# Kernel tuning notes

Measured on AMD Instinct MI355X. Metric: run time of the kernel, lower is better.

## Reference

```python
import jax, jax.numpy as jnp
import numpy as np

N = 20000
E = 320000
D_IN = 256
D = 128
H = 4
L = 2
NUM_CLASSES = 7
LN_EPS = 1e-5


def setup_inputs() -> dict:
    key = jax.random.key(0)
    ks = jax.random.split(key, 12)
    inp = {}
    inp["x"] = jax.random.normal(ks[0], (N, D_IN), dtype=jnp.float32)
    inp["edge_index"] = jax.random.randint(ks[1], (2, E), 0, N, dtype=jnp.int32)
    inp["W_in"] = jax.random.normal(ks[2], (D_IN, D), dtype=jnp.float32) / np.sqrt(D_IN)
    inp["b_in"] = jnp.zeros((D,), jnp.float32)
    inp["Wq"] = jax.random.normal(ks[3], (L, D, H * D), dtype=jnp.float32) / np.sqrt(D)
    inp["bq"] = jnp.zeros((L, H * D), jnp.float32)
    inp["Wk"] = jax.random.normal(ks[4], (L, D, H * D), dtype=jnp.float32) / np.sqrt(D)
    inp["bk"] = jnp.zeros((L, H * D), jnp.float32)
    inp["Wv"] = jax.random.normal(ks[5], (L, D, H * D), dtype=jnp.float32) / np.sqrt(D)
    inp["bv"] = jnp.zeros((L, H * D), jnp.float32)
    inp["Wskip"] = jax.random.normal(ks[6], (L, D, D), dtype=jnp.float32) / np.sqrt(D)
    inp["bskip"] = jnp.zeros((L, D), jnp.float32)
    inp["ln_g"] = jnp.ones((L, D), jnp.float32)
    inp["ln_b"] = jnp.zeros((L, D), jnp.float32)
    inp["Wc"] = jax.random.normal(ks[7], (D, NUM_CLASSES), dtype=jnp.float32) / np.sqrt(D)
    inp["bc"] = jnp.zeros((NUM_CLASSES,), jnp.float32)
    return inp


def degree_pe(edge_index):
    # degree of source nodes (edge_index[0]), then sinusoidal encoding of the degree
    deg = jax.ops.segment_sum(jnp.ones((E,), jnp.float32), edge_index[0], num_segments=N)
    i = jnp.arange(D, dtype=jnp.float32)
    freq = deg[:, None] / jnp.power(10000.0, i / D)[None, :]  # [N, D]
    return jnp.where((jnp.arange(D) % 2 == 0)[None, :], jnp.sin(freq), jnp.cos(freq))


def transformer_conv(xf, edge_index, Wq, bq, Wk, bk, Wv, bv, Wskip, bskip):
    # PyG TransformerConv: heads=H, concat=False (mean over heads), root_weight=True
    src, dst = edge_index[0], edge_index[1]
    q = (xf @ Wq + bq).reshape(N, H, D)
    k = (xf @ Wk + bk).reshape(N, H, D)
    v = (xf @ Wv + bv).reshape(N, H, D)
    qe = q[dst]                        # [E, H, D]
    ke = k[src]
    ve = v[src]
    scores = jnp.sum(qe * ke, axis=-1) / np.sqrt(D)  # [E, H]
    m = jax.ops.segment_max(scores, dst, num_segments=N)        # [N, H]
    p = jnp.exp(scores - m[dst])
    s = jax.ops.segment_sum(p, dst, num_segments=N)              # [N, H]
    alpha = p / (s[dst] + 1e-16)
    agg = jax.ops.segment_sum(alpha[:, :, None] * ve, dst, num_segments=N)  # [N, H, D]
    out = jnp.mean(agg, axis=1)       # concat=False -> average heads
    return out + xf @ Wskip + bskip   # root skip connection


def layer_norm(x, g, b):
    mu = jnp.mean(x, axis=-1, keepdims=True)
    var = jnp.mean(jnp.square(x - mu), axis=-1, keepdims=True)
    return (x - mu) * jax.lax.rsqrt(var + LN_EPS) * g + b


def reference(x, edge_index, W_in, b_in, Wq, bq, Wk, bk, Wv, bv, Wskip, bskip, ln_g, ln_b, Wc, bc):
    h = x @ W_in + b_in
    h = h + degree_pe(edge_index)
    for l in range(L):
        h_new = transformer_conv(h, edge_index, Wq[l], bq[l], Wk[l], bk[l], Wv[l], bv[l], Wskip[l], bskip[l])
        h = layer_norm(h + h_new, ln_g[l], ln_b[l])
        if l < L - 1:
            h = jax.nn.relu(h)
    return h @ Wc + bc  # [N, num_classes]
```

## Files before the change

kernel.cpp:

```cpp
#include <hip/hip_runtime.h>
#include <math.h>

#define NN 20000
#define EE 320000
#define DIN 256
#define DD 128
#define HHEADS 4
#define NCLS 7

typedef __attribute__((ext_vector_type(8))) __bf16 bf16x8;
typedef __attribute__((ext_vector_type(4))) float f32x4;
typedef __attribute__((ext_vector_type(2))) float f32x2;

__device__ __forceinline__ unsigned short f2bf(float f) {
  union { float f; unsigned int u; } c; c.f = f;
  unsigned int r = c.u + 0x7fffu + ((c.u >> 16) & 1u);
  return (unsigned short)(r >> 16);
}
__device__ __forceinline__ __bf16 f2bf16(float f) {
  union { unsigned short u; __bf16 b; } cv; cv.u = f2bf(f); return cv.b;
}
__device__ __forceinline__ unsigned char fp8enc(float v) {
  return (unsigned char)(__builtin_amdgcn_cvt_pk_fp8_f32(v, 0.f, 0, false) & 0xff);
}

__global__ void zero_ints(int* __restrict__ p, int n) {
  int i = blockIdx.x * blockDim.x + threadIdx.x;
  if (i < n) p[i] = 0;
}

__global__ void count_kernel(const int* __restrict__ ei, int* __restrict__ deg_src,
                             int* __restrict__ cnt_dst) {
  int e = blockIdx.x * blockDim.x + threadIdx.x;
  if (e >= EE) return;
  atomicAdd(&deg_src[ei[e]], 1);
  atomicAdd(&cnt_dst[ei[EE + e]], 1);
}

__global__ __launch_bounds__(1024) void scan_kernel(const int* __restrict__ cnt,
                                                    int* __restrict__ row_ptr,
                                                    int* __restrict__ fillp) {
  __shared__ int wsum[16];
  __shared__ int carry_s;
  const int tid = threadIdx.x;
  const int wid = tid >> 6, lane = tid & 63;
  if (tid == 0) carry_s = 0;
  __syncthreads();
  for (int base = 0; base < NN; base += 1024) {
    int i = base + tid;
    int x = (i < NN) ? cnt[i] : 0;
    int v = x;
#pragma unroll
    for (int off = 1; off < 64; off <<= 1) {
      int t = __shfl_up(v, off);
      if (lane >= off) v += t;
    }
    if (lane == 63) wsum[wid] = v;
    __syncthreads();
    int woff = 0;
    for (int w = 0; w < wid; ++w) woff += wsum[w];
    int excl = carry_s + woff + v - x;
    if (i < NN) { row_ptr[i] = excl; fillp[i] = excl; }
    __syncthreads();
    if (tid == 1023) carry_s += woff + v;
    __syncthreads();
  }
  if (tid == 0) row_ptr[NN] = EE;
}

__global__ void scatter_kernel(const int* __restrict__ ei, int* __restrict__ fillp,
                               int* __restrict__ ssrc) {
  int e = blockIdx.x * blockDim.x + threadIdx.x;
  if (e >= EE) return;
  int s = ei[e], d = ei[EE + e];
  int pos = atomicAdd(&fillp[d], 1);
  ssrc[pos] = s;
}

__global__ void pack_weights(const float* __restrict__ W_in, const float* __restrict__ Wq,
                             const float* __restrict__ Wk, const float* __restrict__ Wv,
                             const float* __restrict__ Wsk, const float* __restrict__ Wc,
                             __bf16* __restrict__ WT) {
  int idx = blockIdx.x * blockDim.x + threadIdx.x;
  if (idx >= 460800) return;
  float val;
  if (idx < 32768) {
    int m = idx >> 8, k = idx & 255;
    val = W_in[k * 128 + m];
  } else if (idx < 458752) {
    int t = idx - 32768;
    int l = t / 212992; int t2 = t - l * 212992;
    int r = t2 >> 7, kk = t2 & 127;
    if (r < 512) {
      val = Wq[l * 65536 + kk * 512 + r];
    } else if (r < 1536) {
      int rr = r - 512;
      int b = rr >> 7, cc = rr & 127;
      int dim = b * 64 + (cc & 63);
      val = (cc >= 64) ? Wv[l * 65536 + kk * 512 + dim]
                       : Wk[l * 65536 + kk * 512 + dim];
    } else {
      val = Wsk[l * 16384 + kk * 128 + (r - 1536)];
    }
  } else {
    int t = idx - 458752;
    int r = t >> 7, kk = t & 127;
    val = (r < NCLS) ? Wc[kk * NCLS + r] : 0.f;
  }
  WT[idx] = f2bf16(val);
}

__global__ void pack_bias(const float* __restrict__ bq, const float* __restrict__ bk,
                          const float* __restrict__ bv, const float* __restrict__ bsk,
                          const float* __restrict__ bc, float* __restrict__ bcomb,
                          float* __restrict__ bcpad) {
  int idx = blockIdx.x * blockDim.x + threadIdx.x;
  if (idx < 3328) {
    int l = idx / 1664, r = idx % 1664;
    float v;
    if (r < 512) {
      v = bq[l * 512 + r];
    } else if (r < 1536) {
      int rr = r - 512;
      int b = rr >> 7, cc = rr & 127;
      int dim = b * 64 + (cc & 63);
      v = (cc >= 64) ? bv[l * 512 + dim] : bk[l * 512 + dim];
    } else {
      v = bsk[l * 128 + (r - 1536)];
    }
    bcomb[idx] = v;
  } else if (idx < 3344) {
    int r = idx - 3328;
    bcpad[r] = (r < NCLS) ? bc[r] : 0.f;
  }
}

__global__ __launch_bounds__(256) void mfma_gemm_in(
    const float* __restrict__ A, const __bf16* __restrict__ BT,
    const float* __restrict__ bias, float* __restrict__ o_f32,
    __bf16* __restrict__ o_bf0, const int* __restrict__ deg) {
  constexpr int K = 256;
  __shared__ __attribute__((aligned(16))) __bf16 As[64][136];
  __shared__ __attribute__((aligned(16))) __bf16 Bs[128][136];
  const int tid = threadIdx.x;
  const int brow = blockIdx.x * 64;
  const int wave = tid >> 6, lane = tid & 63;
  const int wm = wave & 1, wn = wave >> 1;
  const int lm = lane & 15, lk = (lane >> 4) * 8;
  const int srow16 = tid >> 4;
  const int sc8 = (tid & 15) * 8;
  f32x4 acc[2][4] = {};
  for (int k0 = 0; k0 < K; k0 += 128) {
    if (k0) __syncthreads();
#pragma unroll
    for (int t = 0; t < 4; ++t) {
      int row = t * 16 + srow16;
      int arow = brow + row;
      arow = (arow < NN) ? arow : (NN - 1);
      const float* ap = A + (size_t)arow * K + k0 + sc8;
      float4 a0 = *(const float4*)ap, a1 = *(const float4*)(ap + 4);
      uint4 w;
      w.x = (unsigned)f2bf(a0.x) | ((unsigned)f2bf(a0.y) << 16);
      w.y = (unsigned)f2bf(a0.z) | ((unsigned)f2bf(a0.w) << 16);
      w.z = (unsigned)f2bf(a1.x) | ((unsigned)f2bf(a1.y) << 16);
      w.w = (unsigned)f2bf(a1.z) | ((unsigned)f2bf(a1.w) << 16);
      *reinterpret_cast<uint4*>(&As[row][sc8]) = w;
    }
#pragma unroll
    for (int t = 0; t < 8; ++t) {
      int row = t * 16 + srow16;
      *reinterpret_cast<uint4*>(&Bs[row][sc8]) =
          *reinterpret_cast<const uint4*>(BT + (size_t)row * K + k0 + sc8);
    }
    __syncthreads();
#pragma unroll
    for (int ks = 0; ks < 4; ++ks) {
      bf16x8 af[2], bfr[4];
#pragma unroll
      for (int i = 0; i < 2; ++i)
        af[i] = *reinterpret_cast<const bf16x8*>(&As[wm * 32 + i * 16 + lm][ks * 32 + lk]);
#pragma unroll
      for (int j = 0; j < 4; ++j)
        bfr[j] = *reinterpret_cast<const bf16x8*>(&Bs[wn * 64 + j * 16 + lm][ks * 32 + lk]);
#pragma unroll
      for (int i = 0; i < 2; ++i)
#pragma unroll
        for (int j = 0; j < 4; ++j)
          acc[i][j] = __builtin_amdgcn_mfma_f32_16x16x32_bf16(af[i], bfr[j], acc[i][j], 0, 0, 0);
    }
  }
#pragma unroll
  for (int i = 0; i < 2; ++i) {
#pragma unroll
    for (int j = 0; j < 4; ++j) {
      const int col = wn * 64 + j * 16 + lm;
      const float bb = bias[col];
#pragma unroll
      for (int r = 0; r < 4; ++r) {
        const int row = brow + wm * 32 + i * 16 + (lane >> 4) * 4 + r;
        if (row >= NN) continue;
        float val = acc[i][j][r] + bb;
        float dg = (float)deg[row];
        float freq = dg * __expf(-0.07195578415606394f * (float)col);
        val += (col & 1) ? __cosf(freq) : __sinf(freq);
        o_f32[(size_t)row * DD + col] = val;
        o_bf0[(size_t)row * DD + col] = f2bf16(val);
      }
    }
  }
}

__global__ __launch_bounds__(512) void mfma_gemm_qkv(
    const __bf16* __restrict__ A, const __bf16* __restrict__ BT,
    const float* __restrict__ bias, const float* __restrict__ resid,
    __bf16* __restrict__ o_q, unsigned char* __restrict__ o_fp8,
    float* __restrict__ o_hs) {
  __shared__ __attribute__((aligned(16))) unsigned char smem[34816];
  auto Bs = reinterpret_cast<__bf16(*)[136]>(smem);

  const int bid = blockIdx.x;
  const int xcd = bid & 7;
  const int jj = bid >> 3;
  const int brow128 = xcd * 20 + (jj % 20);
  if (brow128 * 128 >= NN) return;
  const int brow = brow128 * 128;
  const int bcol = (jj / 20) * 128;

  const int tid = threadIdx.x;
  const int wave = tid >> 6, lane = tid & 63;
  const int wm = wave & 3, wn = wave >> 2;
  const int lm = lane & 15, lk = (lane >> 4) * 8, l4 = (lane >> 4) * 4;
  const int srow32 = tid >> 4;
  const int sc8 = (tid & 15) * 8;

  uint4 breg[4];
#pragma unroll
  for (int t = 0; t < 4; ++t)
    breg[t] = *reinterpret_cast<const uint4*>(BT + (size_t)(bcol + t * 32 + srow32) * 128 + sc8);

  bf16x8 af[2][4];
#pragma unroll
  for (int i = 0; i < 2; ++i) {
    int row = brow + wm * 32 + i * 16 + lm;
    row = (row < NN) ? row : (NN - 1);
    const __bf16* ap = A + (size_t)row * 128 + lk;
#pragma unroll
    for (int ks = 0; ks < 4; ++ks)
      af[i][ks] = *reinterpret_cast<const bf16x8*>(ap + ks * 32);
  }

#pragma unroll
  for (int t = 0; t < 4; ++t)
    *reinterpret_cast<uint4*>(&Bs[t * 32 + srow32][sc8]) = breg[t];
  __syncthreads();

  f32x4 acc[2][4] = {};
#pragma unroll
  for (int ks = 0; ks < 4; ++ks) {
    bf16x8 bfr[4];
#pragma unroll
    for (int j = 0; j < 4; ++j)
      bfr[j] = *reinterpret_cast<const bf16x8*>(&Bs[wn * 64 + j * 16 + lm][ks * 32 + lk]);
#pragma unroll
    for (int i = 0; i < 2; ++i)
#pragma unroll
      for (int j = 0; j < 4; ++j)
        acc[i][j] = __builtin_amdgcn_mfma_f32_16x16x32_bf16(af[i][ks], bfr[j], acc[i][j], 0, 0, 0);
  }

  __syncthreads();

  if (bcol < 512) {
    auto qt = reinterpret_cast<__bf16(*)[136]>(smem);
#pragma unroll
    for (int i = 0; i < 2; ++i)
#pragma unroll
      for (int j = 0; j < 4; ++j) {
        const int cc = wn * 64 + j * 16 + lm;
        const float bb = bias[bcol + cc];
#pragma unroll
        for (int r = 0; r < 4; ++r)
          qt[wm * 32 + i * 16 + l4 + r][cc] = f2bf16(acc[i][j][r] + bb);
      }
    __syncthreads();
#pragma unroll
    for (int p = 0; p < 4; ++p) {
      int slot = tid + p * 512;
      int row = slot >> 4, c = slot & 15;
      int grow = brow + row;
      if (grow < NN)
        *reinterpret_cast<uint4*>(o_q + (size_t)grow * 512 + bcol + c * 8) =
            *reinterpret_cast<const uint4*>(&qt[row][c * 8]);
    }
  } else if (bcol < 1536) {
    auto kt = reinterpret_cast<unsigned char(*)[128]>(smem);
    const int b = (bcol - 512) >> 7;
#pragma unroll
    for (int i = 0; i < 2; ++i)
#pragma unroll
      for (int j = 0; j < 4; ++j) {
        const float bb = bias[bcol + wn * 64 + j * 16 + lm];
        const int boff = (j * 2 + (lm >> 3)) * 16 + wn * 8 + (lm & 7);
#pragma unroll
        for (int r = 0; r < 4; ++r) {
          int lrow = wm * 32 + i * 16 + l4 + r;
          kt[lrow][boff ^ (((lrow >> 2) & 3) << 5)] = fp8enc(acc[i][j][r] + bb);
        }
      }
    __syncthreads();
#pragma unroll
    for (int p = 0; p < 2; ++p) {
      int slot = tid + p * 512;
      int row = slot >> 3, c = slot & 7;
      int grow = brow + row;
      if (grow < NN)
        *reinterpret_cast<uint4*>(o_fp8 + (size_t)grow * 1024 + b * 128 + c * 16) =
            *reinterpret_cast<const uint4*>(&kt[row][(c * 16) ^ (((row >> 2) & 3) << 5)]);
    }
  } else {
#pragma unroll
    for (int i = 0; i < 2; ++i)
#pragma unroll
      for (int j = 0; j < 4; ++j) {
        const int col = bcol + wn * 64 + j * 16 + lm;
        const float bb = bias[col];
#pragma unroll
        for (int r = 0; r < 4; ++r) {
          const int row = brow + wm * 32 + i * 16 + l4 + r;
          if (row >= NN) continue;
          o_hs[(size_t)row * DD + (col - 1536)] =
              acc[i][j][r] + bb + resid[(size_t)row * DD + (col - 1536)];
        }
      }
  }
}

__global__ __launch_bounds__(256) void mfma_gemm_cls(
    const __bf16* __restrict__ A, const __bf16* __restrict__ BT,
    const float* __restrict__ bias, float* __restrict__ out) {
  __shared__ __attribute__((aligned(16))) __bf16 Bs[16][136];
  const int tid = threadIdx.x;
  const int wave = tid >> 6, lane = tid & 63;
  const int lm = lane & 15, lk = (lane >> 4) * 8, l4 = (lane >> 4) * 4;
  const int brow = blockIdx.x * 128 + wave * 32;
  {
    int srow = tid >> 4, sc8 = (tid & 15) * 8;
    *reinterpret_cast<uint4*>(&Bs[srow][sc8]) =
        *reinterpret_cast<const uint4*>(BT + (size_t)srow * 128 + sc8);
  }
  __syncthreads();
  bf16x8 af[2][4];
#pragma unroll
  for (int i = 0; i < 2; ++i) {
    int row = brow + i * 16 + lm;
    row = (row < NN) ? row : (NN - 1);
    const __bf16* ap = A + (size_t)row * 128 + lk;
#pragma unroll
    for (int ks = 0; ks < 4; ++ks) af[i][ks] = *reinterpret_cast<const bf16x8*>(ap + ks * 32);
  }
  f32x4 acc[2] = {};
#pragma unroll
  for (int ks = 0; ks < 4; ++ks) {
    bf16x8 bfr = *reinterpret_cast<const bf16x8*>(&Bs[lm][ks * 32 + lk]);
#pragma unroll
    for (int i = 0; i < 2; ++i)
      acc[i] = __builtin_amdgcn_mfma_f32_16x16x32_bf16(af[i][ks], bfr, acc[i], 0, 0, 0);
  }
  if (lm < NCLS) {
    const float bb = bias[lm];
#pragma unroll
    for (int i = 0; i < 2; ++i) {
#pragma unroll
      for (int r = 0; r < 4; ++r) {
        int row = brow + i * 16 + l4 + r;
        if (row < NN) out[(size_t)row * NCLS + lm] = acc[i][r] + bb;
      }
    }
  }
}

__device__ __forceinline__ uint4 loadkv(const unsigned char* __restrict__ kv,
                                        const int* __restrict__ ssrc, int ee, int lane) {
  return *reinterpret_cast<const uint4*>(kv + (size_t)ssrc[ee] * 1024 + lane * 16);
}
__device__ __forceinline__ float qdot8(const f32x2 (&qv)[4], unsigned kx, unsigned ky) {
  f32x2 kd0 = __builtin_amdgcn_cvt_pk_f32_fp8((int)kx, false);
  f32x2 kd1 = __builtin_amdgcn_cvt_pk_f32_fp8((int)kx, true);
  f32x2 kd2 = __builtin_amdgcn_cvt_pk_f32_fp8((int)ky, false);
  f32x2 kd3 = __builtin_amdgcn_cvt_pk_f32_fp8((int)ky, true);
  f32x2 d2 = qv[0] * kd0;
  d2 = qv[1] * kd1 + d2;
  d2 = qv[2] * kd2 + d2;
  d2 = qv[3] * kd3 + d2;
  float d = d2[0] + d2[1];
  d += __shfl_xor(d, 1);
  d += __shfl_xor(d, 2);
  d += __shfl_xor(d, 4);
  d += __shfl_xor(d, 8);
  return d;
}
__device__ __forceinline__ void accum8(f32x2 (&a)[4], float& m, float& s, float sc,
                                       unsigned vz, unsigned vw) {
  if (sc > m) {
    float c = __expf(m - sc);
    f32x2 c2 = {c, c};
    s *= c;
#pragma unroll
    for (int d = 0; d < 4; ++d) a[d] *= c2;
    m = sc;
  }
  float w = __expf(sc - m);
  s += w;
  f32x2 w2 = {w, w};
  f32x2 vd0 = __builtin_amdgcn_cvt_pk_f32_fp8((int)vz, false);
  f32x2 vd1 = __builtin_amdgcn_cvt_pk_f32_fp8((int)vz, true);
  f32x2 vd2 = __builtin_amdgcn_cvt_pk_f32_fp8((int)vw, false);
  f32x2 vd3 = __builtin_amdgcn_cvt_pk_f32_fp8((int)vw, true);
  a[0] = w2 * vd0 + a[0];
  a[1] = w2 * vd1 + a[1];
  a[2] = w2 * vd2 + a[2];
  a[3] = w2 * vd3 + a[3];
}

__global__ __launch_bounds__(256) void attn_fused(
    const __bf16* __restrict__ qb, const unsigned char* __restrict__ kv,
    const float* __restrict__ hs,
    const int* __restrict__ row_ptr, const int* __restrict__ ssrc,
    const float* __restrict__ ln_g, const float* __restrict__ ln_b,
    float* __restrict__ h_out, __bf16* __restrict__ hb_out, int relu_flag) {
  const int node = blockIdx.x * 4 + (threadIdx.x >> 6);
  const int lane = threadIdx.x & 63;
  const int grp = lane >> 4, l16 = lane & 15;
  const int e0 = row_ptr[node], e1 = row_ptr[node + 1];
  const float scale = 0.088388347648318447f;

  f32x2 qv[4];
  {
    uint4 qw = *reinterpret_cast<const uint4*>(qb + (size_t)node * 512 + lane * 8);
    union { unsigned u; float f; } c;
    c.u = qw.x << 16; qv[0][0] = c.f; c.u = qw.x & 0xffff0000u; qv[0][1] = c.f;
    c.u = qw.y << 16; qv[1][0] = c.f; c.u = qw.y & 0xffff0000u; qv[1][1] = c.f;
    c.u = qw.z << 16; qv[2][0] = c.f; c.u = qw.z & 0xffff0000u; qv[2][1] = c.f;
    c.u = qw.w << 16; qv[3][0] = c.f; c.u = qw.w & 0xffff0000u; qv[3][1] = c.f;
  }
  float m = -INFINITY, s = 0.f;
  f32x2 a[4] = {};

  uint4 w0, w1, w2, w3;
  if (e0 + 0 < e1) w0 = loadkv(kv, ssrc, e0 + 0, lane);
  if (e0 + 1 < e1) w1 = loadkv(kv, ssrc, e0 + 1, lane);
  if (e0 + 2 < e1) w2 = loadkv(kv, ssrc, e0 + 2, lane);
  if (e0 + 3 < e1) w3 = loadkv(kv, ssrc, e0 + 3, lane);
  int e = e0;
  while (e < e1) {
    {
      float sc = qdot8(qv, w0.x, w0.y) * scale;
      unsigned vz = w0.z, vw = w0.w;
      if (e + 4 < e1) w0 = loadkv(kv, ssrc, e + 4, lane);
      accum8(a, m, s, sc, vz, vw);
    }
    if (e + 1 < e1) {
      float sc = qdot8(qv, w1.x, w1.y) * scale;
      unsigned vz = w1.z, vw = w1.w;
      if (e + 5 < e1) w1 = loadkv(kv, ssrc, e + 5, lane);
      accum8(a, m, s, sc, vz, vw);
    }
    if (e + 2 < e1) {
      float sc = qdot8(qv, w2.x, w2.y) * scale;
      unsigned vz = w2.z, vw = w2.w;
      if (e + 6 < e1) w2 = loadkv(kv, ssrc, e + 6, lane);
      accum8(a, m, s, sc, vz, vw);
    }
    if (e + 3 < e1) {
      float sc = qdot8(qv, w3.x, w3.y) * scale;
      unsigned vz = w3.z, vw = w3.w;
      if (e + 7 < e1) w3 = loadkv(kv, ssrc, e + 7, lane);
      accum8(a, m, s, sc, vz, vw);
    }
    e += 4;
  }

  float inv = 0.25f / (s + 1e-16f);
  float am[8];
#pragma unroll
  for (int d = 0; d < 8; ++d) {
    float ad = a[d >> 1][d & 1] * inv;
    ad += __shfl_xor(ad, 16);
    ad += __shfl_xor(ad, 32);
    am[d] = ad;
  }

  const float4* hp = reinterpret_cast<const float4*>(hs + (size_t)node * DD + l16 * 8);
  float4 h0 = hp[0], h1 = hp[1];
  float val[8];
  val[0] = am[0] + h0.x; val[1] = am[1] + h0.y; val[2] = am[2] + h0.z; val[3] = am[3] + h0.w;
  val[4] = am[4] + h1.x; val[5] = am[5] + h1.y; val[6] = am[6] + h1.z; val[7] = am[7] + h1.w;
  float sum = 0.f, sq = 0.f;
#pragma unroll
  for (int d = 0; d < 8; ++d) { sum += val[d]; sq += val[d] * val[d]; }
  sum += __shfl_xor(sum, 1); sq += __shfl_xor(sq, 1);
  sum += __shfl_xor(sum, 2); sq += __shfl_xor(sq, 2);
  sum += __shfl_xor(sum, 4); sq += __shfl_xor(sq, 4);
  sum += __shfl_xor(sum, 8); sq += __shfl_xor(sq, 8);
  float mu = sum * (1.f / 128.f);
  float var = sq * (1.f / 128.f) - mu * mu;
  float rstd = rsqrtf(var + 1e-5f);

  const float4* gp = reinterpret_cast<const float4*>(ln_g + l16 * 8);
  const float4* bp = reinterpret_cast<const float4*>(ln_b + l16 * 8);
  float4 g0 = gp[0], g1 = gp[1];
  float4 b0 = bp[0], b1 = bp[1];
  float y[8];
  y[0] = (val[0] - mu) * rstd * g0.x + b0.x;
  y[1] = (val[1] - mu) * rstd * g0.y + b0.y;
  y[2] = (val[2] - mu) * rstd * g0.z + b0.z;
  y[3] = (val[3] - mu) * rstd * g0.w + b0.w;
  y[4] = (val[4] - mu) * rstd * g1.x + b1.x;
  y[5] = (val[5] - mu) * rstd * g1.y + b1.y;
  y[6] = (val[6] - mu) * rstd * g1.z + b1.z;
  y[7] = (val[7] - mu) * rstd * g1.w + b1.w;
  if (relu_flag) {
#pragma unroll
    for (int d = 0; d < 8; ++d) y[d] = fmaxf(y[d], 0.f);
  }
  if (grp == 0) {
    float4* op = reinterpret_cast<float4*>(h_out + (size_t)node * DD + l16 * 8);
    op[0] = make_float4(y[0], y[1], y[2], y[3]);
    op[1] = make_float4(y[4], y[5], y[6], y[7]);
  } else if (grp == 1) {
    uint4 w;
    w.x = (unsigned)f2bf(y[0]) | ((unsigned)f2bf(y[1]) << 16);
    w.y = (unsigned)f2bf(y[2]) | ((unsigned)f2bf(y[3]) << 16);
    w.z = (unsigned)f2bf(y[4]) | ((unsigned)f2bf(y[5]) << 16);
    w.w = (unsigned)f2bf(y[6]) | ((unsigned)f2bf(y[7]) << 16);
    *reinterpret_cast<uint4*>(hb_out + (size_t)node * DD + l16 * 8) = w;
  }
}

extern "C" void kernel_launch(void* const* d_in, const int* in_sizes, int n_in,
                              void* d_out, int out_size, void* d_ws, size_t ws_size,
                              hipStream_t stream) {
  const float* x    = (const float*)d_in[0];
  const int*   ei   = (const int*)d_in[1];
  const float* W_in = (const float*)d_in[2];
  const float* b_in = (const float*)d_in[3];
  const float* Wq   = (const float*)d_in[4];
  const float* bq   = (const float*)d_in[5];
  const float* Wk   = (const float*)d_in[6];
  const float* bk   = (const float*)d_in[7];
  const float* Wv   = (const float*)d_in[8];
  const float* bv   = (const float*)d_in[9];
  const float* Wsk  = (const float*)d_in[10];
  const float* bsk  = (const float*)d_in[11];
  const float* ln_g = (const float*)d_in[12];
  const float* ln_b = (const float*)d_in[13];
  const float* Wc   = (const float*)d_in[14];
  const float* bc   = (const float*)d_in[15];
  float* out = (float*)d_out;

  char* ws = (char*)d_ws;
  size_t off = 0;
  float*  hA    = (float*)(ws + off);  off += (size_t)NN * DD * 4;
  float*  hB    = (float*)(ws + off);  off += (size_t)NN * DD * 4;
  __bf16* qb    = (__bf16*)(ws + off); off += (size_t)NN * 512 * 2;
  unsigned char* kvb = (unsigned char*)(ws + off); off += (size_t)NN * 1024;
  float*  hsb   = (float*)(ws + off);  off += (size_t)NN * DD * 4;
  __bf16* hb0   = (__bf16*)(ws + off); off += (size_t)NN * DD * 2;
  __bf16* hb1   = (__bf16*)(ws + off); off += (size_t)NN * DD * 2;
  __bf16* WT    = (__bf16*)(ws + off); off += (size_t)460800 * 2;
  float*  bcomb = (float*)(ws + off);  off += (size_t)3328 * 4;
  float*  bcpad = (float*)(ws + off);  off += (size_t)16 * 4;
  int* deg      = (int*)(ws + off);    off += (size_t)NN * 4;
  int* cnt      = (int*)(ws + off);    off += (size_t)NN * 4;
  int* fillp    = (int*)(ws + off);    off += (size_t)NN * 4;
  int* row_ptr  = (int*)(ws + off);    off += (size_t)(NN + 1) * 4;
  int* ssrc     = (int*)(ws + off);    off += (size_t)EE * 4;

  __bf16* W_inT = WT;
  __bf16* W2T   = WT + 32768;
  __bf16* WcT   = WT + 458752;

  zero_ints<<<(2 * NN + 255) / 256, 256, 0, stream>>>(deg, 2 * NN);
  count_kernel<<<(EE + 255) / 256, 256, 0, stream>>>(ei, deg, cnt);
  scan_kernel<<<1, 1024, 0, stream>>>(cnt, row_ptr, fillp);
  scatter_kernel<<<(EE + 255) / 256, 256, 0, stream>>>(ei, fillp, ssrc);

  pack_weights<<<(460800 + 255) / 256, 256, 0, stream>>>(W_in, Wq, Wk, Wv, Wsk, Wc, WT);
  pack_bias<<<(3344 + 255) / 256, 256, 0, stream>>>(bq, bk, bv, bsk, bc, bcomb, bcpad);

  mfma_gemm_in<<<dim3((NN + 63) / 64, 1), 256, 0, stream>>>(x, W_inT, b_in, hA, hb0, deg);

  const float*  h_in_l[2]   = {hA, hB};
  float*        h_out_l[2]  = {hB, hA};
  const __bf16* hb_in_l[2]  = {hb0, hb1};
  __bf16*       hb_out_l[2] = {hb1, hb0};

  for (int l = 0; l < 2; ++l) {
    mfma_gemm_qkv<<<2080, 512, 0, stream>>>(hb_in_l[l], W2T + (size_t)l * 212992,
                                            bcomb + (size_t)l * 1664, h_in_l[l],
                                            qb, kvb, hsb);
    attn_fused<<<NN / 4, 256, 0, stream>>>(qb, kvb, hsb, row_ptr, ssrc,
                                           ln_g + (size_t)l * DD, ln_b + (size_t)l * DD,
                                           h_out_l[l], hb_out_l[l], (l == 0) ? 1 : 0);
  }

  mfma_gemm_cls<<<dim3((NN + 127) / 128, 1), 256, 0, stream>>>(hb0, WcT, bcpad, out);
}
```

Baseline: 290.7 us.

## Process attention nodes in descending in-degree order for load balancing

Adds a counting-sort pass (histogram, reverse scan, scatter) that orders nodes by in-degree, heaviest first, and makes the fused attention kernel map each wavefront to a node through this order. The aim is less tail imbalance: blocks of four nodes now hold nodes of similar degree, and the long nodes are scheduled early. The cost is three extra small kernel launches and scattered, non-contiguous node accesses to q, h and the output rows.

```diff
diff --git a/kernel.cpp b/kernel.cpp
--- a/kernel.cpp
+++ b/kernel.cpp
@@ -75,6 +75,37 @@
   int s = ei[e], d = ei[EE + e];
   int pos = atomicAdd(&fillp[d], 1);
   ssrc[pos] = s;
+}
+
+__global__ void hist_kernel(const int* __restrict__ cnt, int* __restrict__ hist) {
+  int i = blockIdx.x * blockDim.x + threadIdx.x;
+  if (i < NN) atomicAdd(&hist[min(cnt[i], 255)], 1);
+}
+__global__ void hscan_kernel(const int* __restrict__ hist, int* __restrict__ binfill) {
+  const int tid = threadIdx.x;
+  const int rd = 255 - tid;
+  const int lane = tid & 63, wid = tid >> 6;
+  __shared__ int wsum[4];
+  int x = hist[rd];
+  int v = x;
+#pragma unroll
+  for (int off = 1; off < 64; off <<= 1) {
+    int t = __shfl_up(v, off);
+    if (lane >= off) v += t;
+  }
+  if (lane == 63) wsum[wid] = v;
+  __syncthreads();
+  int woff = 0;
+  for (int w = 0; w < wid; ++w) woff += wsum[w];
+  binfill[rd] = woff + v - x;
+}
+__global__ void fill_order_kernel(const int* __restrict__ cnt, int* __restrict__ binfill,
+                                  int* __restrict__ order) {
+  int i = blockIdx.x * blockDim.x + threadIdx.x;
+  if (i >= NN) return;
+  int d = min(cnt[i], 255);
+  int pos = atomicAdd(&binfill[d], 1);
+  order[pos] = i;
 }
 
 __global__ void pack_weights(const float* __restrict__ W_in, const float* __restrict__ Wq,
@@ -424,11 +455,11 @@
 
 __global__ __launch_bounds__(256) void attn_fused(
     const __bf16* __restrict__ qb, const unsigned char* __restrict__ kv,
-    const float* __restrict__ hs,
+    const float* __restrict__ hs, const int* __restrict__ order,
     const int* __restrict__ row_ptr, const int* __restrict__ ssrc,
     const float* __restrict__ ln_g, const float* __restrict__ ln_b,
     float* __restrict__ h_out, __bf16* __restrict__ hb_out, int relu_flag) {
-  const int node = blockIdx.x * 4 + (threadIdx.x >> 6);
+  const int node = order[blockIdx.x * 4 + (threadIdx.x >> 6)];
   const int lane = threadIdx.x & 63;
   const int grp = lane >> 4, l16 = lane & 15;
   const int e0 = row_ptr[node], e1 = row_ptr[node + 1];
@@ -572,18 +603,25 @@
   float*  bcpad = (float*)(ws + off);  off += (size_t)16 * 4;
   int* deg      = (int*)(ws + off);    off += (size_t)NN * 4;
   int* cnt      = (int*)(ws + off);    off += (size_t)NN * 4;
+  int* hist     = (int*)(ws + off);    off += (size_t)256 * 4;
+  int* binfill  = (int*)(ws + off);    off += (size_t)256 * 4;
   int* fillp    = (int*)(ws + off);    off += (size_t)NN * 4;
   int* row_ptr  = (int*)(ws + off);    off += (size_t)(NN + 1) * 4;
   int* ssrc     = (int*)(ws + off);    off += (size_t)EE * 4;
+  int* order    = (int*)(ws + off);    off += (size_t)NN * 4;
 
   __bf16* W_inT = WT;
   __bf16* W2T   = WT + 32768;
   __bf16* WcT   = WT + 458752;
 
-  zero_ints<<<(2 * NN + 255) / 256, 256, 0, stream>>>(deg, 2 * NN);
+  zero_ints<<<(2 * NN + 512 + 255) / 256, 256, 0, stream>>>(deg, 2 * NN + 512);
   count_kernel<<<(EE + 255) / 256, 256, 0, stream>>>(ei, deg, cnt);
   scan_kernel<<<1, 1024, 0, stream>>>(cnt, row_ptr, fillp);
   scatter_kernel<<<(EE + 255) / 256, 256, 0, stream>>>(ei, fillp, ssrc);
+
+  hist_kernel<<<(NN + 255) / 256, 256, 0, stream>>>(cnt, hist);
+  hscan_kernel<<<1, 256, 0, stream>>>(hist, binfill);
+  fill_order_kernel<<<(NN + 255) / 256, 256, 0, stream>>>(cnt, binfill, order);
 
   pack_weights<<<(460800 + 255) / 256, 256, 0, stream>>>(W_in, Wq, Wk, Wv, Wsk, Wc, WT);
   pack_bias<<<(3344 + 255) / 256, 256, 0, stream>>>(bq, bk, bv, bsk, bc, bcomb, bcpad);
@@ -599,7 +637,7 @@
     mfma_gemm_qkv<<<2080, 512, 0, stream>>>(hb_in_l[l], W2T + (size_t)l * 212992,
                                             bcomb + (size_t)l * 1664, h_in_l[l],
                                             qb, kvb, hsb);
-    attn_fused<<<NN / 4, 256, 0, stream>>>(qb, kvb, hsb, row_ptr, ssrc,
+    attn_fused<<<NN / 4, 256, 0, stream>>>(qb, kvb, hsb, order, row_ptr, ssrc,
                                            ln_g + (size_t)l * DD, ln_b + (size_t)l * DD,
                                            h_out_l[l], hb_out_l[l], (l == 0) ? 1 : 0);
   }
```

Result: slower. 369.7 us (+27.2%).
